# Optimization experiments

Measured on AMD Instinct MI355X. Metric: run time of the kernel, lower is better.

Reference implementation:

```python
import jax, jax.numpy as jnp
import numpy as np

DIM = 1024
NB = 25            # num_basis_functions
ALPHA_X = 1.0
DT = 0.001
MAX_TIME = 10.0
TAU = 1.0
ALPHA_Y = 25.0
BETA_Y = 6.25
WEIGHT_SCALE = 1000.0
T = int(MAX_TIME / DT) + 1   # rollout buffer length = 10001


def setup_inputs() -> dict:
    key = jax.random.key(0)
    k1, k2, k3 = jax.random.split(key, 3)
    y0 = jax.random.normal(k1, (DIM,), dtype=jnp.float32)
    # learned parameters of the module
    g = jax.random.normal(k2, (DIM,), dtype=jnp.float32)
    weights = jax.random.normal(k3, (DIM, NB), dtype=jnp.float32) / NB
    return {"y0": y0, "g": g, "weights": weights}


def reference(y0, g, weights):
    # basis function centers / widths (canonical system)
    c = jnp.exp(-ALPHA_X * jnp.linspace(0.0, MAX_TIME, NB)).astype(y0.dtype)
    h = (NB / c).astype(y0.dtype)
    decay = jnp.asarray(1.0 - ALPHA_X * TAU * DT, y0.dtype)

    def step(carry, _):
        x, y, dy = carry
        x = x * decay                                   # decay_time()
        psi = jnp.exp(-h * (x - c) ** 2)                # [NB]
        # force(y0): sum over basis functions, per dim
        force = (WEIGHT_SCALE * (weights @ psi)) * x * (g - y0) / jnp.sum(psi)  # [DIM]
        ddy = ALPHA_Y * (BETA_Y * (g - y) - dy) + force
        ndy = dy + TAU * DT * ddy
        ny = y + TAU * DT * ndy
        return (x, ny, ndy), jnp.concatenate([ny, ndy])

    x0 = jnp.asarray(1.0, y0.dtype)
    dy0 = jnp.zeros_like(y0)
    _, rows = jax.lax.scan(step, (x0, y0, dy0), None, length=T - 1)  # [T-1, 2*DIM]
    first = jnp.concatenate([y0, dy0])[None]                          # [1, 2*DIM]
    ydy = jnp.concatenate([first, rows], axis=0)                      # [T, 2*DIM]
    y0rep = jnp.broadcast_to(y0, (T, DIM))
    return jnp.concatenate([y0rep, ydy], axis=1)                      # [T, 3*DIM]
```

## Files before the change

### kernel.cpp

```cpp
#include <hip/hip_runtime.h>
#include <math.h>


#define DIM    1024
#define NB     25
#define NSTEP  10000
#define CHUNKS 250
#define LSTEPS 40
#define SC     25
#define SS     10
#define QS     32

__global__ __launch_bounds__(64) void k_prep(float* __restrict__ q,
                                             float* __restrict__ QY,
                                             float* __restrict__ QD,
                                             float* __restrict__ WT,
                                             const float* __restrict__ W,
                                             double logdecay,
                                             double a00, double a01,
                                             double a10, double a11) {
    const int c = blockIdx.x;
    const int tid = threadIdx.x;
    if (c >= CHUNKS) {
        int k = c - CHUNKS;
        for (int d = tid; d < DIM; d += 64)
            WT[k * DIM + d] = W[d * NB + k];
        return;
    }
    __shared__ float lq[LSTEPS][NB + 1];
    if (tid < LSTEPS) {
        int t = c * LSTEPS + tid + 1;
        float x = (float)exp((double)t * logdecay);
        float psi[NB];
        float S = 0.f;
#pragma unroll
        for (int k = 0; k < NB; ++k) {
            float lk = (10.0f / 24.0f) * (float)k;
            float ck = expf(-lk);
            float hk = 25.0f / ck;
            float dxc = x - ck;
            float p = expf(-hk * dxc * dxc);
            psi[k] = p;
            S += p;
        }
        float scale = 1000.0f * x / S;
        float* qrow = q + (size_t)(c * LSTEPS + tid) * QS;
#pragma unroll
        for (int k = 0; k < NB; ++k) {
            float v = psi[k] * scale;
            qrow[k] = v;
            lq[tid][k] = v;
        }
    }
    __syncthreads();
    if (tid < NB) {
        double py = (double)0.001f * (double)0.001f;
        double pd = (double)0.001f;
        double qy = 0.0, qd = 0.0;
        for (int j = LSTEPS - 1; j >= 0; --j) {
            double v = (double)lq[j][tid];
            qy += py * v;
            qd += pd * v;
            double npy = a00 * py + a01 * pd;
            double npd = a10 * py + a11 * pd;
            py = npy; pd = npd;
        }
        QY[c * QS + tid] = (float)qy;
        QD[c * QS + tid] = (float)qd;
    }
}

__global__ __launch_bounds__(256) void k_dots(const float* __restrict__ QY,
                                              const float* __restrict__ QD,
                                              const float* __restrict__ WT,
                                              const float* __restrict__ g,
                                              const float* __restrict__ y0,
                                              float* __restrict__ dots,
                                              double spY, double spD) {
    const int idx = blockIdx.x * 256 + threadIdx.x;
    const int d = idx & (DIM - 1);
    const int c = idx >> 10;
    const float gd  = g[d];
    const float gd0 = gd - y0[d];
    float sy = 0.f, sd = 0.f;
#pragma unroll
    for (int k = 0; k < NB; ++k) {
        float wk = WT[k * DIM + d];
        sy += wk * QY[c * QS + k];
        sd += wk * QD[c * QS + k];
    }
    dots[c * DIM + d]                = (float)((double)gd * spY + (double)gd0 * (double)sy);
    dots[CHUNKS * DIM + c * DIM + d] = (float)((double)gd * spD + (double)gd0 * (double)sd);
}

__global__ __launch_bounds__(256) void k_scanA(const float* __restrict__ dots,
                                               float* __restrict__ usY,
                                               float* __restrict__ usD,
                                               double m00, double m01,
                                               double m10, double m11) {
    const int idx = blockIdx.x * 256 + threadIdx.x;
    const int d = idx & (DIM - 1);
    const int s = idx >> 10;
    double vy = 0.0, vdy = 0.0;
#pragma unroll
    for (int i = 0; i < SS; ++i) {
        int c = s * SS + i;
        double ry = (double)dots[c * DIM + d];
        double rd = (double)dots[CHUNKS * DIM + c * DIM + d];
        double ny  = m00 * vy + m01 * vdy + ry;
        double ndy = m10 * vy + m11 * vdy + rd;
        vy = ny; vdy = ndy;
    }
    usY[s * DIM + d] = (float)vy;
    usD[s * DIM + d] = (float)vdy;
}

__global__ __launch_bounds__(256) void k_scanB(const float* __restrict__ usY,
                                               const float* __restrict__ usD,
                                               const float* __restrict__ y0,
                                               float* __restrict__ ssY,
                                               float* __restrict__ ssD,
                                               double b00, double b01,
                                               double b10, double b11) {
    const int d = blockIdx.x * 256 + threadIdx.x;
    float uy[SC], ud[SC];
#pragma unroll
    for (int s = 0; s < SC; ++s) {
        uy[s] = usY[s * DIM + d];
        ud[s] = usD[s * DIM + d];
    }
    double vy = (double)y0[d], vdy = 0.0;
#pragma unroll
    for (int s = 0; s < SC; ++s) {
        ssY[s * DIM + d] = (float)vy;
        ssD[s * DIM + d] = (float)vdy;
        double ny  = b00 * vy + b01 * vdy + (double)uy[s];
        double ndy = b10 * vy + b11 * vdy + (double)ud[s];
        vy = ny; vdy = ndy;
    }
}

__global__ __launch_bounds__(256) void k_scanC(const float* __restrict__ dots,
                                               const float* __restrict__ ssY,
                                               const float* __restrict__ ssD,
                                               float* __restrict__ vs,
                                               double m00, double m01,
                                               double m10, double m11) {
    const int idx = blockIdx.x * 256 + threadIdx.x;
    const int d = idx & (DIM - 1);
    const int s = idx >> 10;
    double vy = (double)ssY[s * DIM + d];
    double vdy = (double)ssD[s * DIM + d];
#pragma unroll
    for (int i = 0; i < SS; ++i) {
        int c = s * SS + i;
        vs[c * DIM + d] = (float)vy;
        vs[CHUNKS * DIM + c * DIM + d] = (float)vdy;
        double ry = (double)dots[c * DIM + d];
        double rd = (double)dots[CHUNKS * DIM + c * DIM + d];
        double ny  = m00 * vy + m01 * vdy + ry;
        double ndy = m10 * vy + m11 * vdy + rd;
        vy = ny; vdy = ndy;
    }
}

__global__ __launch_bounds__(256) void k_roll(const float* __restrict__ q,
                                              const float* __restrict__ WT,
                                              const float* __restrict__ g,
                                              const float* __restrict__ y0,
                                              const float* __restrict__ vs,
                                              float* __restrict__ out) {
    __shared__ float lq[LSTEPS][QS];
    const int c = blockIdx.y;
    const int tid = threadIdx.x;
    const int d = blockIdx.x * 256 + tid;
    {
        const float4* src = (const float4*)(q + (size_t)c * LSTEPS * QS);
        float4* dst = (float4*)&lq[0][0];
        for (int i = tid; i < LSTEPS * (QS / 4); i += 256) dst[i] = src[i];
    }
    float w[NB];
#pragma unroll
    for (int k = 0; k < NB; ++k) w[k] = WT[k * DIM + d];
    const float y0d = y0[d];
    const float gd  = g[d];
    const float gd0 = gd - y0d;
    float y  = vs[c * DIM + d];
    float dy = vs[CHUNKS * DIM + c * DIM + d];
    __syncthreads();
    if (c == 0) {
        out[d] = y0d;
        out[DIM + d] = y0d;
        out[2 * DIM + d] = 0.f;
    }
    float* op = out + (size_t)(c * LSTEPS + 1) * (3 * DIM);
#pragma unroll 2
    for (int j = 0; j < LSTEPS; ++j) {
        const float4* row = (const float4*)&lq[j][0];
        float dot = 0.f;
#pragma unroll
        for (int m = 0; m < 6; ++m) {
            float4 qv = row[m];
            dot += w[4 * m + 0] * qv.x;
            dot += w[4 * m + 1] * qv.y;
            dot += w[4 * m + 2] * qv.z;
            dot += w[4 * m + 3] * qv.w;
        }
        dot += w[24] * lq[j][24];
        float f   = dot * gd0;
        float ddy = 25.0f * (6.25f * (gd - y) - dy) + f;
        dy = dy + 0.001f * ddy;
        y  = y + 0.001f * dy;
        op[d] = y0d;
        op[DIM + d] = y;
        op[2 * DIM + d] = dy;
        op += 3 * DIM;
    }
}

extern "C" void kernel_launch(void* const* d_in, const int* in_sizes, int n_in,
                              void* d_out, int out_size, void* d_ws, size_t ws_size,
                              hipStream_t stream) {
    const float* y0 = (const float*)d_in[0];
    const float* g  = (const float*)d_in[1];
    const float* W  = (const float*)d_in[2];
    float* out = (float*)d_out;

    float* q   = (float*)d_ws;
    float* QY  = q   + (size_t)NSTEP * QS;
    float* QD  = QY  + (size_t)CHUNKS * QS;
    float* WT  = QD  + (size_t)CHUNKS * QS;
    float* usY = WT  + (size_t)NB * DIM;
    float* usD = usY + (size_t)SC * DIM;
    float* ssY = usD + (size_t)SC * DIM;
    float* ssD = ssY + (size_t)SC * DIM;
    float* vs  = ssD + (size_t)SC * DIM;
    float* dots = out;

    const double dtD = (double)0.001f;
    const double aD = 25.0, abD = 25.0 * 6.25;
    const double a00 = 1.0 - dtD * dtD * abD;
    const double a01 = dtD * (1.0 - dtD * aD);
    const double a10 = -dtD * abD;
    const double a11 = 1.0 - dtD * aD;
    double m00 = 1, m01 = 0, m10 = 0, m11 = 1;
    double py = dtD * dtD, pd = dtD, sY = 0.0, sD = 0.0;
    for (int i = 0; i < LSTEPS; ++i) {
        double t00 = a00 * m00 + a01 * m10;
        double t01 = a00 * m01 + a01 * m11;
        double t10 = a10 * m00 + a11 * m10;
        double t11 = a10 * m01 + a11 * m11;
        m00 = t00; m01 = t01; m10 = t10; m11 = t11;
        sY += py; sD += pd;
        double npy = a00 * py + a01 * pd;
        double npd = a10 * py + a11 * pd;
        py = npy; pd = npd;
    }
    double b00 = 1, b01 = 0, b10 = 0, b11 = 1;
    for (int i = 0; i < SS; ++i) {
        double t00 = m00 * b00 + m01 * b10;
        double t01 = m00 * b01 + m01 * b11;
        double t10 = m10 * b00 + m11 * b10;
        double t11 = m10 * b01 + m11 * b11;
        b00 = t00; b01 = t01; b10 = t10; b11 = t11;
    }
    const double spY = 156.25 * sY;
    const double spD = 156.25 * sD;
    const double logdecay = log((double)(1.0f - 0.001f));

    k_prep<<<CHUNKS + NB, 64, 0, stream>>>(q, QY, QD, WT, W, logdecay, a00, a01, a10, a11);
    k_dots<<<(DIM * CHUNKS) / 256, 256, 0, stream>>>(QY, QD, WT, g, y0, dots, spY, spD);
    k_scanA<<<(DIM * SC) / 256, 256, 0, stream>>>(dots, usY, usD, m00, m01, m10, m11);
    k_scanB<<<DIM / 256, 256, 0, stream>>>(usY, usD, y0, ssY, ssD, b00, b01, b10, b11);
    k_scanC<<<(DIM * SC) / 256, 256, 0, stream>>>(dots, ssY, ssD, vs, m00, m01, m10, m11);
    k_roll<<<dim3(DIM / 256, CHUNKS), 256, 0, stream>>>(q, WT, g, y0, vs, out);
}
```

Measured before the change: 152.8 us.

## Stage rollout rows in LDS for coalesced float4 stores and fuse scan stages

```diff
diff --git a/kernel.cpp b/kernel.cpp
--- a/kernel.cpp
+++ b/kernel.cpp
@@ -5,10 +5,10 @@
 #define DIM    1024
 #define NB     25
 #define NSTEP  10000
-#define CHUNKS 250
-#define LSTEPS 40
+#define CHUNKS 500
+#define LSTEPS 20
 #define SC     25
-#define SS     10
+#define SS     20
 #define QS     32
 
 __global__ __launch_bounds__(64) void k_prep(float* __restrict__ q,
@@ -51,6 +51,8 @@
             qrow[k] = v;
             lq[tid][k] = v;
         }
+#pragma unroll
+        for (int k = NB; k < QS; ++k) qrow[k] = 0.f;
     }
     __syncthreads();
     if (tid < NB) {
@@ -102,7 +104,7 @@
     const int d = idx & (DIM - 1);
     const int s = idx >> 10;
     double vy = 0.0, vdy = 0.0;
-#pragma unroll
+#pragma unroll 4
     for (int i = 0; i < SS; ++i) {
         int c = s * SS + i;
         double ry = (double)dots[c * DIM + d];
@@ -115,43 +117,27 @@
     usD[s * DIM + d] = (float)vdy;
 }
 
-__global__ __launch_bounds__(256) void k_scanB(const float* __restrict__ usY,
-                                               const float* __restrict__ usD,
-                                               const float* __restrict__ y0,
-                                               float* __restrict__ ssY,
-                                               float* __restrict__ ssD,
-                                               double b00, double b01,
-                                               double b10, double b11) {
-    const int d = blockIdx.x * 256 + threadIdx.x;
-    float uy[SC], ud[SC];
-#pragma unroll
-    for (int s = 0; s < SC; ++s) {
-        uy[s] = usY[s * DIM + d];
-        ud[s] = usD[s * DIM + d];
-    }
+__global__ __launch_bounds__(256) void k_scanBC(const float* __restrict__ dots,
+                                                const float* __restrict__ usY,
+                                                const float* __restrict__ usD,
+                                                const float* __restrict__ y0,
+                                                float* __restrict__ vs,
+                                                double m00, double m01,
+                                                double m10, double m11,
+                                                double b00, double b01,
+                                                double b10, double b11) {
+    const int b = blockIdx.x;
+    const int s = b >> 2;
+    const int d = (b & 3) * 256 + threadIdx.x;
     double vy = (double)y0[d], vdy = 0.0;
-#pragma unroll
-    for (int s = 0; s < SC; ++s) {
-        ssY[s * DIM + d] = (float)vy;
-        ssD[s * DIM + d] = (float)vdy;
-        double ny  = b00 * vy + b01 * vdy + (double)uy[s];
-        double ndy = b10 * vy + b11 * vdy + (double)ud[s];
+    for (int i = 0; i < s; ++i) {
+        double uy = (double)usY[i * DIM + d];
+        double ud = (double)usD[i * DIM + d];
+        double ny  = b00 * vy + b01 * vdy + uy;
+        double ndy = b10 * vy + b11 * vdy + ud;
         vy = ny; vdy = ndy;
     }
-}
-
-__global__ __launch_bounds__(256) void k_scanC(const float* __restrict__ dots,
-                                               const float* __restrict__ ssY,
-                                               const float* __restrict__ ssD,
-                                               float* __restrict__ vs,
-                                               double m00, double m01,
-                                               double m10, double m11) {
-    const int idx = blockIdx.x * 256 + threadIdx.x;
-    const int d = idx & (DIM - 1);
-    const int s = idx >> 10;
-    double vy = (double)ssY[s * DIM + d];
-    double vdy = (double)ssD[s * DIM + d];
-#pragma unroll
+#pragma unroll 4
     for (int i = 0; i < SS; ++i) {
         int c = s * SS + i;
         vs[c * DIM + d] = (float)vy;
@@ -164,57 +150,80 @@
     }
 }
 
-__global__ __launch_bounds__(256) void k_roll(const float* __restrict__ q,
+__global__ __launch_bounds__(512) void k_roll(const float* __restrict__ q,
                                               const float* __restrict__ WT,
                                               const float* __restrict__ g,
                                               const float* __restrict__ y0,
                                               const float* __restrict__ vs,
                                               float* __restrict__ out) {
     __shared__ float lq[LSTEPS][QS];
-    const int c = blockIdx.y;
+    __shared__ float rowY[2][DIM];
+    __shared__ float rowD[2][DIM];
+    const int c = blockIdx.x;
     const int tid = threadIdx.x;
-    const int d = blockIdx.x * 256 + tid;
-    {
-        const float4* src = (const float4*)(q + (size_t)c * LSTEPS * QS);
-        float4* dst = (float4*)&lq[0][0];
-        for (int i = tid; i < LSTEPS * (QS / 4); i += 256) dst[i] = src[i];
-    }
-    float w[NB];
-#pragma unroll
-    for (int k = 0; k < NB; ++k) w[k] = WT[k * DIM + d];
-    const float y0d = y0[d];
-    const float gd  = g[d];
-    const float gd0 = gd - y0d;
-    float y  = vs[c * DIM + d];
-    float dy = vs[CHUNKS * DIM + c * DIM + d];
+    const int d0 = tid;
+    const int d1 = tid + 512;
+    if (tid < LSTEPS * QS / 4)
+        ((float4*)&lq[0][0])[tid] = ((const float4*)(q + (size_t)c * LSTEPS * QS))[tid];
+
+    float w0[NB], w1[NB];
+#pragma unroll
+    for (int k = 0; k < NB; ++k) {
+        w0[k] = WT[k * DIM + d0];
+        w1[k] = WT[k * DIM + d1];
+    }
+    const float g0 = g[d0], g1 = g[d1];
+    const float gd00 = g0 - y0[d0], gd01 = g1 - y0[d1];
+    float y_0  = vs[c * DIM + d0];
+    float y_1  = vs[c * DIM + d1];
+    float dy_0 = vs[CHUNKS * DIM + c * DIM + d0];
+    float dy_1 = vs[CHUNKS * DIM + c * DIM + d1];
+    float4 y0q = make_float4(0.f, 0.f, 0.f, 0.f);
+    if (tid < 256) y0q = ((const float4*)y0)[tid];
+
+    if (c == 0) {
+        float4* o = (float4*)out;
+        if (tid < 256) {
+            o[tid]       = y0q;
+            o[256 + tid] = y0q;
+            o[512 + tid] = make_float4(0.f, 0.f, 0.f, 0.f);
+        }
+    }
     __syncthreads();
-    if (c == 0) {
-        out[d] = y0d;
-        out[DIM + d] = y0d;
-        out[2 * DIM + d] = 0.f;
-    }
-    float* op = out + (size_t)(c * LSTEPS + 1) * (3 * DIM);
-#pragma unroll 2
+
+    float* base = out + (size_t)(c * LSTEPS + 1) * (3 * DIM);
     for (int j = 0; j < LSTEPS; ++j) {
         const float4* row = (const float4*)&lq[j][0];
-        float dot = 0.f;
+        float dot0 = 0.f, dot1 = 0.f;
 #pragma unroll
         for (int m = 0; m < 6; ++m) {
             float4 qv = row[m];
-            dot += w[4 * m + 0] * qv.x;
-            dot += w[4 * m + 1] * qv.y;
-            dot += w[4 * m + 2] * qv.z;
-            dot += w[4 * m + 3] * qv.w;
-        }
-        dot += w[24] * lq[j][24];
-        float f   = dot * gd0;
-        float ddy = 25.0f * (6.25f * (gd - y) - dy) + f;
-        dy = dy + 0.001f * ddy;
-        y  = y + 0.001f * dy;
-        op[d] = y0d;
-        op[DIM + d] = y;
-        op[2 * DIM + d] = dy;
-        op += 3 * DIM;
+            dot0 += w0[4 * m + 0] * qv.x; dot1 += w1[4 * m + 0] * qv.x;
+            dot0 += w0[4 * m + 1] * qv.y; dot1 += w1[4 * m + 1] * qv.y;
+            dot0 += w0[4 * m + 2] * qv.z; dot1 += w1[4 * m + 2] * qv.z;
+            dot0 += w0[4 * m + 3] * qv.w; dot1 += w1[4 * m + 3] * qv.w;
+        }
+        float q24 = lq[j][24];
+        dot0 += w0[24] * q24;
+        dot1 += w1[24] * q24;
+        float f0 = dot0 * gd00, f1 = dot1 * gd01;
+        float ddy0 = 25.0f * (6.25f * (g0 - y_0) - dy_0) + f0;
+        float ddy1 = 25.0f * (6.25f * (g1 - y_1) - dy_1) + f1;
+        dy_0 = dy_0 + 0.001f * ddy0;
+        dy_1 = dy_1 + 0.001f * ddy1;
+        y_0  = y_0 + 0.001f * dy_0;
+        y_1  = y_1 + 0.001f * dy_1;
+        const int pb = j & 1;
+        rowY[pb][d0] = y_0;  rowY[pb][d1] = y_1;
+        rowD[pb][d0] = dy_0; rowD[pb][d1] = dy_1;
+        __syncthreads();
+        float4* op = (float4*)(base + (size_t)j * (3 * DIM));
+        if (tid < 256) {
+            op[tid]       = y0q;
+            op[512 + tid] = *(const float4*)&rowD[pb][tid * 4];
+        } else {
+            op[tid]       = *(const float4*)&rowY[pb][(tid - 256) * 4];
+        }
     }
 }
 
@@ -232,9 +241,7 @@
     float* WT  = QD  + (size_t)CHUNKS * QS;
     float* usY = WT  + (size_t)NB * DIM;
     float* usD = usY + (size_t)SC * DIM;
-    float* ssY = usD + (size_t)SC * DIM;
-    float* ssD = ssY + (size_t)SC * DIM;
-    float* vs  = ssD + (size_t)SC * DIM;
+    float* vs  = usD + (size_t)SC * DIM;
     float* dots = out;
 
     const double dtD = (double)0.001f;
@@ -271,7 +278,7 @@
     k_prep<<<CHUNKS + NB, 64, 0, stream>>>(q, QY, QD, WT, W, logdecay, a00, a01, a10, a11);
     k_dots<<<(DIM * CHUNKS) / 256, 256, 0, stream>>>(QY, QD, WT, g, y0, dots, spY, spD);
     k_scanA<<<(DIM * SC) / 256, 256, 0, stream>>>(dots, usY, usD, m00, m01, m10, m11);
-    k_scanB<<<DIM / 256, 256, 0, stream>>>(usY, usD, y0, ssY, ssD, b00, b01, b10, b11);
-    k_scanC<<<(DIM * SC) / 256, 256, 0, stream>>>(dots, ssY, ssD, vs, m00, m01, m10, m11);
-    k_roll<<<dim3(DIM / 256, CHUNKS), 256, 0, stream>>>(q, WT, g, y0, vs, out);
-}
+    k_scanBC<<<SC * 4, 256, 0, stream>>>(dots, usY, usD, y0, vs, m00, m01, m10, m11,
+                                         b00, b01, b10, b11);
+    k_roll<<<CHUNKS, 512, 0, stream>>>(q, WT, g, y0, vs, out);
+}
```

New measurement: 162.5 us. 1.06x slower.

## Fuse dot products into chunk scans and merge middle scan stages

Applied to the files above, without the earlier changes.

```diff
diff --git a/kernel.cpp b/kernel.cpp
--- a/kernel.cpp
+++ b/kernel.cpp
@@ -70,43 +70,35 @@
     }
 }
 
-__global__ __launch_bounds__(256) void k_dots(const float* __restrict__ QY,
+__global__ __launch_bounds__(256) void k_midA(const float* __restrict__ QY,
                                               const float* __restrict__ QD,
                                               const float* __restrict__ WT,
                                               const float* __restrict__ g,
                                               const float* __restrict__ y0,
-                                              float* __restrict__ dots,
-                                              double spY, double spD) {
-    const int idx = blockIdx.x * 256 + threadIdx.x;
-    const int d = idx & (DIM - 1);
-    const int c = idx >> 10;
+                                              float* __restrict__ usY,
+                                              float* __restrict__ usD,
+                                              double spY, double spD,
+                                              double m00, double m01,
+                                              double m10, double m11) {
+    const int b = blockIdx.x;
+    const int s = b >> 2;
+    const int d = (b & 3) * 256 + threadIdx.x;
+    float w[NB];
+#pragma unroll
+    for (int k = 0; k < NB; ++k) w[k] = WT[k * DIM + d];
     const float gd  = g[d];
     const float gd0 = gd - y0[d];
-    float sy = 0.f, sd = 0.f;
-#pragma unroll
-    for (int k = 0; k < NB; ++k) {
-        float wk = WT[k * DIM + d];
-        sy += wk * QY[c * QS + k];
-        sd += wk * QD[c * QS + k];
-    }
-    dots[c * DIM + d]                = (float)((double)gd * spY + (double)gd0 * (double)sy);
-    dots[CHUNKS * DIM + c * DIM + d] = (float)((double)gd * spD + (double)gd0 * (double)sd);
-}
-
-__global__ __launch_bounds__(256) void k_scanA(const float* __restrict__ dots,
-                                               float* __restrict__ usY,
-                                               float* __restrict__ usD,
-                                               double m00, double m01,
-                                               double m10, double m11) {
-    const int idx = blockIdx.x * 256 + threadIdx.x;
-    const int d = idx & (DIM - 1);
-    const int s = idx >> 10;
     double vy = 0.0, vdy = 0.0;
-#pragma unroll
     for (int i = 0; i < SS; ++i) {
         int c = s * SS + i;
-        double ry = (double)dots[c * DIM + d];
-        double rd = (double)dots[CHUNKS * DIM + c * DIM + d];
+        float sy = 0.f, sd = 0.f;
+#pragma unroll
+        for (int k = 0; k < NB; ++k) {
+            sy += w[k] * QY[c * QS + k];
+            sd += w[k] * QD[c * QS + k];
+        }
+        double ry = (double)(float)((double)gd * spY + (double)gd0 * (double)sy);
+        double rd = (double)(float)((double)gd * spD + (double)gd0 * (double)sd);
         double ny  = m00 * vy + m01 * vdy + ry;
         double ndy = m10 * vy + m11 * vdy + rd;
         vy = ny; vdy = ndy;
@@ -115,49 +107,47 @@
     usD[s * DIM + d] = (float)vdy;
 }
 
-__global__ __launch_bounds__(256) void k_scanB(const float* __restrict__ usY,
-                                               const float* __restrict__ usD,
-                                               const float* __restrict__ y0,
-                                               float* __restrict__ ssY,
-                                               float* __restrict__ ssD,
-                                               double b00, double b01,
-                                               double b10, double b11) {
-    const int d = blockIdx.x * 256 + threadIdx.x;
-    float uy[SC], ud[SC];
-#pragma unroll
-    for (int s = 0; s < SC; ++s) {
-        uy[s] = usY[s * DIM + d];
-        ud[s] = usD[s * DIM + d];
-    }
+__global__ __launch_bounds__(256) void k_midB(const float* __restrict__ QY,
+                                              const float* __restrict__ QD,
+                                              const float* __restrict__ WT,
+                                              const float* __restrict__ g,
+                                              const float* __restrict__ y0,
+                                              const float* __restrict__ usY,
+                                              const float* __restrict__ usD,
+                                              float* __restrict__ vs,
+                                              double spY, double spD,
+                                              double m00, double m01,
+                                              double m10, double m11,
+                                              double b00, double b01,
+                                              double b10, double b11) {
+    const int b = blockIdx.x;
+    const int s = b >> 2;
+    const int d = (b & 3) * 256 + threadIdx.x;
+    float w[NB];
+#pragma unroll
+    for (int k = 0; k < NB; ++k) w[k] = WT[k * DIM + d];
+    const float gd  = g[d];
+    const float gd0 = gd - y0[d];
     double vy = (double)y0[d], vdy = 0.0;
-#pragma unroll
-    for (int s = 0; s < SC; ++s) {
-        ssY[s * DIM + d] = (float)vy;
-        ssD[s * DIM + d] = (float)vdy;
-        double ny  = b00 * vy + b01 * vdy + (double)uy[s];
-        double ndy = b10 * vy + b11 * vdy + (double)ud[s];
+    for (int i = 0; i < s; ++i) {
+        double uy = (double)usY[i * DIM + d];
+        double ud = (double)usD[i * DIM + d];
+        double ny  = b00 * vy + b01 * vdy + uy;
+        double ndy = b10 * vy + b11 * vdy + ud;
         vy = ny; vdy = ndy;
     }
-}
-
-__global__ __launch_bounds__(256) void k_scanC(const float* __restrict__ dots,
-                                               const float* __restrict__ ssY,
-                                               const float* __restrict__ ssD,
-                                               float* __restrict__ vs,
-                                               double m00, double m01,
-                                               double m10, double m11) {
-    const int idx = blockIdx.x * 256 + threadIdx.x;
-    const int d = idx & (DIM - 1);
-    const int s = idx >> 10;
-    double vy = (double)ssY[s * DIM + d];
-    double vdy = (double)ssD[s * DIM + d];
-#pragma unroll
     for (int i = 0; i < SS; ++i) {
         int c = s * SS + i;
         vs[c * DIM + d] = (float)vy;
         vs[CHUNKS * DIM + c * DIM + d] = (float)vdy;
-        double ry = (double)dots[c * DIM + d];
-        double rd = (double)dots[CHUNKS * DIM + c * DIM + d];
+        float sy = 0.f, sd = 0.f;
+#pragma unroll
+        for (int k = 0; k < NB; ++k) {
+            sy += w[k] * QY[c * QS + k];
+            sd += w[k] * QD[c * QS + k];
+        }
+        double ry = (double)(float)((double)gd * spY + (double)gd0 * (double)sy);
+        double rd = (double)(float)((double)gd * spD + (double)gd0 * (double)sd);
         double ny  = m00 * vy + m01 * vdy + ry;
         double ndy = m10 * vy + m11 * vdy + rd;
         vy = ny; vdy = ndy;
@@ -232,10 +222,7 @@
     float* WT  = QD  + (size_t)CHUNKS * QS;
     float* usY = WT  + (size_t)NB * DIM;
     float* usD = usY + (size_t)SC * DIM;
-    float* ssY = usD + (size_t)SC * DIM;
-    float* ssD = ssY + (size_t)SC * DIM;
-    float* vs  = ssD + (size_t)SC * DIM;
-    float* dots = out;
+    float* vs  = usD + (size_t)SC * DIM;
 
     const double dtD = (double)0.001f;
     const double aD = 25.0, abD = 25.0 * 6.25;
@@ -269,9 +256,10 @@
     const double logdecay = log((double)(1.0f - 0.001f));
 
     k_prep<<<CHUNKS + NB, 64, 0, stream>>>(q, QY, QD, WT, W, logdecay, a00, a01, a10, a11);
-    k_dots<<<(DIM * CHUNKS) / 256, 256, 0, stream>>>(QY, QD, WT, g, y0, dots, spY, spD);
-    k_scanA<<<(DIM * SC) / 256, 256, 0, stream>>>(dots, usY, usD, m00, m01, m10, m11);
-    k_scanB<<<DIM / 256, 256, 0, stream>>>(usY, usD, y0, ssY, ssD, b00, b01, b10, b11);
-    k_scanC<<<(DIM * SC) / 256, 256, 0, stream>>>(dots, ssY, ssD, vs, m00, m01, m10, m11);
+    k_midA<<<SC * 4, 256, 0, stream>>>(QY, QD, WT, g, y0, usY, usD,
+                                       spY, spD, m00, m01, m10, m11);
+    k_midB<<<SC * 4, 256, 0, stream>>>(QY, QD, WT, g, y0, usY, usD, vs,
+                                       spY, spD, m00, m01, m10, m11,
+                                       b00, b01, b10, b11);
     k_roll<<<dim3(DIM / 256, CHUNKS), 256, 0, stream>>>(q, WT, g, y0, vs, out);
 }
```

New measurement: 160.3 us. 1.05x slower.
